# Performance work log

Measured on AMD Instinct MI355X. Metric: run time of the kernel, lower is better.

Reference implementation:

```python
import jax, jax.numpy as jnp
import numpy as np

B, HW, L, D = 4, 4096, 32, 128
H, DH = 2, 64            # heads, dim_head; inner_dim = H*DH = 128
SCALE = DH ** -0.5


def setup_inputs() -> dict:
    key = jax.random.key(0)
    ks = jax.random.split(key, 6)
    inner = H * DH
    return {
        "x": jax.random.normal(ks[0], (B, HW, 1, D), dtype=jnp.float32),
        "context": jax.random.normal(ks[1], (B, HW, L, D), dtype=jnp.float32),
        "Wq": jax.random.normal(ks[2], (D, inner), dtype=jnp.float32) * 0.02,
        "Wkv": jax.random.normal(ks[3], (D, 2 * inner), dtype=jnp.float32) * 0.02,
        "Wo": jax.random.normal(ks[4], (inner, D), dtype=jnp.float32) * 0.02,
        "bo": jnp.zeros((D,), dtype=jnp.float32),
    }


def reference(x, context, Wq, Wkv, Wo, bo):
    # q: [B, HW, 1, H*DH] -> [B, HW, H, DH] (single query per pixel)
    q = (x @ Wq).reshape(B, HW, H, DH)
    kv = context @ Wkv                       # [B, HW, L, 2*H*DH]
    k, v = jnp.split(kv, 2, axis=-1)
    k = k.reshape(B, HW, L, H, DH)
    v = v.reshape(B, HW, L, H, DH)
    # per-pixel 1xL attention, fused over (B, HW, H)
    sim = jnp.einsum('bphd,bplhd->bphl', q, k) * SCALE   # [B, HW, H, L]
    attn = jax.nn.softmax(sim, axis=-1)
    out = jnp.einsum('bphl,bplhd->bphd', attn, v)        # [B, HW, H, DH]
    out = out.reshape(B, HW, 1, H * DH)
    return out @ Wo + bo                                 # [B, HW, 1, D]
```

## Files before the change

kernel.cpp:

```cpp
#include <hip/hip_runtime.h>

#define NPIX 16384
#define LCTX 32
#define DIM  128
#define SCALE 0.125f

__global__ __launch_bounds__(256)
void fold_kernel(const float* __restrict__ Wq, const float* __restrict__ Wkv,
                 const float* __restrict__ Wo,
                 float* __restrict__ Ms, float* __restrict__ Nf)
{
    const int t = threadIdx.x;
    const int b = blockIdx.x;
    if (b < 128) {
        const int e = b, h = t >> 7, c = t & 127;
        const float4* q4p = reinterpret_cast<const float4*>(Wq + e * 128 + h * 64);
        const float4* k4p = reinterpret_cast<const float4*>(Wkv + c * 256 + h * 64);
        float acc = 0.f;
        #pragma unroll
        for (int d4 = 0; d4 < 16; ++d4) {
            const float4 a = q4p[d4], k = k4p[d4];
            acc += a.x * k.x + a.y * k.y + a.z * k.z + a.w * k.w;
        }
        Ms[e * 256 + t] = SCALE * acc;
    } else {
        const int b2 = b - 128;
        const int i = b2 * 2 + (t >> 7), j = t & 127;
        const int h = i >> 7, c = i & 127;
        const float4* v4p = reinterpret_cast<const float4*>(Wkv + c * 256 + 128 + h * 64);
        float acc = 0.f;
        #pragma unroll
        for (int d4 = 0; d4 < 16; ++d4) {
            const float4 v4 = v4p[d4];
            acc += v4.x * Wo[(h * 64 + d4 * 4 + 0) * 128 + j];
            acc += v4.y * Wo[(h * 64 + d4 * 4 + 1) * 128 + j];
            acc += v4.z * Wo[(h * 64 + d4 * 4 + 2) * 128 + j];
            acc += v4.w * Wo[(h * 64 + d4 * 4 + 3) * 128 + j];
        }
        Nf[i * 128 + j] = acc;
    }
}

__global__ __launch_bounds__(256, 4)
void fused_kernel(const float* __restrict__ x, const float* __restrict__ ctx,
                  const float* __restrict__ Ms, const float* __restrict__ Nf,
                  const float* __restrict__ bo, float* __restrict__ out)
{
    __shared__ float xs[16 * 128];
    __shared__ float cs[16 * 256];

    const int t = threadIdx.x;
    const int w = t >> 6, lane = t & 63;
    const int c0 = lane & 31;
    const int lh = lane >> 5;
    const int pxbase = blockIdx.x * 16;
    const int wpx = pxbase + w * 4;

    #pragma unroll
    for (int k = 0; k < 2; ++k)
        reinterpret_cast<float4*>(xs)[t + k * 256] =
            reinterpret_cast<const float4*>(x + (size_t)pxbase * DIM)[t + k * 256];
    __syncthreads();

    float4 qk4[4];
    #pragma unroll
    for (int p = 0; p < 4; ++p) qk4[p] = make_float4(0.f, 0.f, 0.f, 0.f);
    {
        const float4* ms4 = reinterpret_cast<const float4*>(Ms) + (lh * 32 + c0);
        const float4* xw  = reinterpret_cast<const float4*>(xs + (w * 4) * DIM);
        for (int e4 = 0; e4 < 32; ++e4) {
            float4 xv[4];
            #pragma unroll
            for (int p = 0; p < 4; ++p) xv[p] = xw[p * 32 + e4];
            #pragma unroll
            for (int d = 0; d < 4; ++d) {
                const float4 m4 = ms4[(e4 * 4 + d) * 64];
                #pragma unroll
                for (int p = 0; p < 4; ++p) {
                    const float xe = (d == 0) ? xv[p].x : (d == 1) ? xv[p].y
                                   : (d == 2) ? xv[p].z : xv[p].w;
                    qk4[p].x += xe * m4.x; qk4[p].y += xe * m4.y;
                    qk4[p].z += xe * m4.z; qk4[p].w += xe * m4.w;
                }
            }
        }
    }

    float m[4], dn[4];
    float4 acc[4];
    #pragma unroll
    for (int p = 0; p < 4; ++p) {
        m[p] = -3.0e38f; dn[p] = 0.f;
        acc[p] = make_float4(0.f, 0.f, 0.f, 0.f);
    }
    {
        const float4* cb0 = reinterpret_cast<const float4*>(ctx + (size_t)(wpx + 0) * LCTX * DIM) + c0;
        const float4* cb1 = reinterpret_cast<const float4*>(ctx + (size_t)(wpx + 1) * LCTX * DIM) + c0;
        const float4* cb2 = reinterpret_cast<const float4*>(ctx + (size_t)(wpx + 2) * LCTX * DIM) + c0;
        const float4* cb3 = reinterpret_cast<const float4*>(ctx + (size_t)(wpx + 3) * LCTX * DIM) + c0;
        #pragma unroll 4
        for (int r = 0; r < LCTX; ++r) {
            float4 cv[4];
            cv[0] = cb0[r * 32]; cv[1] = cb1[r * 32];
            cv[2] = cb2[r * 32]; cv[3] = cb3[r * 32];
            float part[4];
            #pragma unroll
            for (int p = 0; p < 4; ++p)
                part[p] = cv[p].x * qk4[p].x + cv[p].y * qk4[p].y
                        + cv[p].z * qk4[p].z + cv[p].w * qk4[p].w;
            #pragma unroll
            for (int off = 16; off >= 1; off >>= 1) {
                #pragma unroll
                for (int p = 0; p < 4; ++p) part[p] += __shfl_xor(part[p], off);
            }
            #pragma unroll
            for (int p = 0; p < 4; ++p) {
                const float mn = fmaxf(m[p], part[p]);
                const float sc = __expf(m[p] - mn);
                const float er = __expf(part[p] - mn);
                dn[p] = dn[p] * sc + er;
                acc[p].x = acc[p].x * sc + er * cv[p].x;
                acc[p].y = acc[p].y * sc + er * cv[p].y;
                acc[p].z = acc[p].z * sc + er * cv[p].z;
                acc[p].w = acc[p].w * sc + er * cv[p].w;
                m[p] = mn;
            }
        }
    }
    {
        float* csw = cs + (w * 4) * 256;
        #pragma unroll
        for (int p = 0; p < 4; ++p) {
            const float inv = 1.f / dn[p];
            float4 r = acc[p];
            r.x *= inv; r.y *= inv; r.z *= inv; r.w *= inv;
            reinterpret_cast<float4*>(csw + p * 256)[lh * 32 + c0] = r;
        }
    }

    {
        const int jq = lane & 31;
        const int ph = lane >> 5;
        const float4* csv0 = reinterpret_cast<const float4*>(cs + (w * 4 + ph * 2 + 0) * 256);
        const float4* csv1 = reinterpret_cast<const float4*>(cs + (w * 4 + ph * 2 + 1) * 256);
        const float4* nf4 = reinterpret_cast<const float4*>(Nf) + jq;
        float4 o0 = make_float4(0.f, 0.f, 0.f, 0.f);
        float4 o1 = make_float4(0.f, 0.f, 0.f, 0.f);
        #pragma unroll 4
        for (int i4 = 0; i4 < 64; ++i4) {
            const float4 a0 = csv0[i4];
            const float4 a1 = csv1[i4];
            #pragma unroll
            for (int d = 0; d < 4; ++d) {
                const float4 n4 = nf4[(i4 * 4 + d) * 32];
                const float a0e = (d == 0) ? a0.x : (d == 1) ? a0.y : (d == 2) ? a0.z : a0.w;
                const float a1e = (d == 0) ? a1.x : (d == 1) ? a1.y : (d == 2) ? a1.z : a1.w;
                o0.x += a0e * n4.x; o0.y += a0e * n4.y; o0.z += a0e * n4.z; o0.w += a0e * n4.w;
                o1.x += a1e * n4.x; o1.y += a1e * n4.y; o1.z += a1e * n4.z; o1.w += a1e * n4.w;
            }
        }
        const float4 b4 = reinterpret_cast<const float4*>(bo)[jq];
        o0.x += b4.x; o0.y += b4.y; o0.z += b4.z; o0.w += b4.w;
        o1.x += b4.x; o1.y += b4.y; o1.z += b4.z; o1.w += b4.w;
        reinterpret_cast<float4*>(out + (size_t)(wpx + ph * 2 + 0) * DIM)[jq] = o0;
        reinterpret_cast<float4*>(out + (size_t)(wpx + ph * 2 + 1) * DIM)[jq] = o1;
    }
}

#define PPB 8
__global__ __launch_bounds__(256, 4)
void ppca_kernel(const float* __restrict__ x, const float* __restrict__ ctx,
                 const float* __restrict__ Wq, const float* __restrict__ Wkv,
                 const float* __restrict__ Wo, const float* __restrict__ bo,
                 float* __restrict__ out)
{
    __shared__ float smem[4096];
    float* xs    = smem;
    float* qs    = smem + 1024;
    float* qks   = smem + 2048;
    float* attns = smem;
    float* ctxws = smem + 2048;
    float* outs  = smem + 1024;

    const int t = threadIdx.x;
    const int gbase = blockIdx.x * PPB;

    reinterpret_cast<float4*>(xs)[t] =
        reinterpret_cast<const float4*>(x + (size_t)gbase * DIM)[t];
    __syncthreads();

    {
        const int j = t & 127, pg = t >> 7;
        float acc[4] = {0.f, 0.f, 0.f, 0.f};
        for (int k = 0; k < 32; ++k) {
            const float w0 = Wq[(4*k + 0) * DIM + j];
            const float w1 = Wq[(4*k + 1) * DIM + j];
            const float w2 = Wq[(4*k + 2) * DIM + j];
            const float w3 = Wq[(4*k + 3) * DIM + j];
            #pragma unroll
            for (int pp = 0; pp < 4; ++pp) {
                const float4 xv = reinterpret_cast<const float4*>(xs + (pg*4 + pp) * DIM)[k];
                acc[pp] += xv.x*w0 + xv.y*w1 + xv.z*w2 + xv.w*w3;
            }
        }
        #pragma unroll
        for (int pp = 0; pp < 4; ++pp) qs[(pg*4 + pp) * DIM + j] = acc[pp];
    }
    __syncthreads();

    {
        const int c = t & 127, h = t >> 7;
        float acc[PPB] = {0.f,0.f,0.f,0.f,0.f,0.f,0.f,0.f};
        const float4* wrow = reinterpret_cast<const float4*>(Wkv + c * 256 + h * 64);
        for (int k = 0; k < 16; ++k) {
            const float4 w4 = wrow[k];
            #pragma unroll
            for (int p = 0; p < PPB; ++p) {
                const float4 q4 = reinterpret_cast<const float4*>(qs + p * DIM + h * 64)[k];
                acc[p] += q4.x*w4.x + q4.y*w4.y + q4.z*w4.z + q4.w*w4.w;
            }
        }
        #pragma unroll
        for (int p = 0; p < PPB; ++p) qks[(p*2 + h) * DIM + c] = acc[p];
    }
    __syncthreads();

    {
        const int l = t & 31, p = t >> 5;
        const float4* cr = reinterpret_cast<const float4*>(ctx + ((size_t)(gbase + p) * LCTX + l) * DIM);
        const float4* q0 = reinterpret_cast<const float4*>(qks + (p*2 + 0) * DIM);
        const float4* q1 = reinterpret_cast<const float4*>(qks + (p*2 + 1) * DIM);
        float s0 = 0.f, s1 = 0.f;
        #pragma unroll 8
        for (int k = 0; k < 32; ++k) {
            const float4 cv = cr[k], a = q0[k], b = q1[k];
            s0 += cv.x*a.x + cv.y*a.y + cv.z*a.z + cv.w*a.w;
            s1 += cv.x*b.x + cv.y*b.y + cv.z*b.z + cv.w*b.w;
        }
        s0 *= SCALE; s1 *= SCALE;
        float m0 = s0, m1 = s1;
        #pragma unroll
        for (int off = 16; off >= 1; off >>= 1) {
            m0 = fmaxf(m0, __shfl_xor(m0, off));
            m1 = fmaxf(m1, __shfl_xor(m1, off));
        }
        const float e0 = __expf(s0 - m0), e1 = __expf(s1 - m1);
        float d0 = e0, d1 = e1;
        #pragma unroll
        for (int off = 16; off >= 1; off >>= 1) {
            d0 += __shfl_xor(d0, off);
            d1 += __shfl_xor(d1, off);
        }
        attns[(p*2 + 0) * LCTX + l] = e0 / d0;
        attns[(p*2 + 1) * LCTX + l] = e1 / d1;
    }
    __syncthreads();

    {
        const int c = t & 127, pg = t >> 7;
        #pragma unroll
        for (int pp = 0; pp < 4; ++pp) {
            const int p = pg*4 + pp;
            const float* cb = ctx + (size_t)(gbase + p) * LCTX * DIM + c;
            const float4* a0p = reinterpret_cast<const float4*>(attns + (p*2 + 0) * LCTX);
            const float4* a1p = reinterpret_cast<const float4*>(attns + (p*2 + 1) * LCTX);
            float s0 = 0.f, s1 = 0.f;
            #pragma unroll
            for (int q = 0; q < 8; ++q) {
                const float4 a0 = a0p[q], a1 = a1p[q];
                const float c0 = cb[(size_t)(4*q + 0) * DIM];
                const float c1 = cb[(size_t)(4*q + 1) * DIM];
                const float c2 = cb[(size_t)(4*q + 2) * DIM];
                const float c3 = cb[(size_t)(4*q + 3) * DIM];
                s0 += a0.x*c0 + a0.y*c1 + a0.z*c2 + a0.w*c3;
                s1 += a1.x*c0 + a1.y*c1 + a1.z*c2 + a1.w*c3;
            }
            ctxws[(p*2 + 0) * DIM + c] = s0;
            ctxws[(p*2 + 1) * DIM + c] = s1;
        }
    }
    __syncthreads();

    {
        const int i = t & 127, pg = t >> 7, h = i >> 6;
        float acc[4] = {0.f, 0.f, 0.f, 0.f};
        for (int k = 0; k < 32; ++k) {
            const float w0 = Wkv[(4*k + 0) * 256 + 128 + i];
            const float w1 = Wkv[(4*k + 1) * 256 + 128 + i];
            const float w2 = Wkv[(4*k + 2) * 256 + 128 + i];
            const float w3 = Wkv[(4*k + 3) * 256 + 128 + i];
            #pragma unroll
            for (int pp = 0; pp < 4; ++pp) {
                const float4 cw = reinterpret_cast<const float4*>(ctxws + ((pg*4 + pp)*2 + h) * DIM)[k];
                acc[pp] += cw.x*w0 + cw.y*w1 + cw.z*w2 + cw.w*w3;
            }
        }
        #pragma unroll
        for (int pp = 0; pp < 4; ++pp) outs[(pg*4 + pp) * DIM + i] = acc[pp];
    }
    __syncthreads();

    {
        const int j = t & 127, pg = t >> 7;
        float acc[4] = {0.f, 0.f, 0.f, 0.f};
        for (int k = 0; k < 32; ++k) {
            const float w0 = Wo[(4*k + 0) * DIM + j];
            const float w1 = Wo[(4*k + 1) * DIM + j];
            const float w2 = Wo[(4*k + 2) * DIM + j];
            const float w3 = Wo[(4*k + 3) * DIM + j];
            #pragma unroll
            for (int pp = 0; pp < 4; ++pp) {
                const float4 ov = reinterpret_cast<const float4*>(outs + (pg*4 + pp) * DIM)[k];
                acc[pp] += ov.x*w0 + ov.y*w1 + ov.z*w2 + ov.w*w3;
            }
        }
        const float bj = bo[j];
        #pragma unroll
        for (int pp = 0; pp < 4; ++pp)
            out[(size_t)(gbase + pg*4 + pp) * DIM + j] = acc[pp] + bj;
    }
}

extern "C" void kernel_launch(void* const* d_in, const int* in_sizes, int n_in,
                              void* d_out, int out_size, void* d_ws, size_t ws_size,
                              hipStream_t stream) {
    const float* x   = (const float*)d_in[0];
    const float* ctx = (const float*)d_in[1];
    const float* Wq  = (const float*)d_in[2];
    const float* Wkv = (const float*)d_in[3];
    const float* Wo  = (const float*)d_in[4];
    const float* bo  = (const float*)d_in[5];
    float* out = (float*)d_out;

    const size_t needed = (size_t)(32768 + 32768) * sizeof(float);
    if (ws_size < needed) {
        dim3 grid(NPIX / PPB), block(256);
        hipLaunchKernelGGL(ppca_kernel, grid, block, 0, stream,
                           x, ctx, Wq, Wkv, Wo, bo, out);
        return;
    }

    float* Ms = (float*)d_ws;
    float* Nf = Ms + 32768;

    hipLaunchKernelGGL(fold_kernel,  dim3(256),  dim3(256), 0, stream, Wq, Wkv, Wo, Ms, Nf);
    hipLaunchKernelGGL(fused_kernel, dim3(NPIX / 16), dim3(256), 0, stream,
                       x, ctx, Ms, Nf, bo, out);
}
```

Baseline: 117.5 us.

## Restructure fused attention kernel to process one pixel at a time per wave

```diff
diff --git a/kernel.cpp b/kernel.cpp
--- a/kernel.cpp
+++ b/kernel.cpp
@@ -4,6 +4,7 @@
 #define LCTX 32
 #define DIM  128
 #define SCALE 0.125f
+#define PXW  4
 
 __global__ __launch_bounds__(256)
 void fold_kernel(const float* __restrict__ Wq, const float* __restrict__ Wkv,
@@ -42,41 +43,33 @@
 }
 
 __global__ __launch_bounds__(256, 4)
-void fused_kernel(const float* __restrict__ x, const float* __restrict__ ctx,
-                  const float* __restrict__ Ms, const float* __restrict__ Nf,
-                  const float* __restrict__ bo, float* __restrict__ out)
+void fused2_kernel(const float* __restrict__ x, const float* __restrict__ ctx,
+                   const float* __restrict__ Ms, const float* __restrict__ Nf,
+                   const float* __restrict__ bo, float* __restrict__ out)
 {
-    __shared__ float xs[16 * 128];
-    __shared__ float cs[16 * 256];
+    __shared__ float cw[4][PXW * 256];
 
     const int t = threadIdx.x;
     const int w = t >> 6, lane = t & 63;
     const int c0 = lane & 31;
-    const int lh = lane >> 5;
-    const int pxbase = blockIdx.x * 16;
-    const int wpx = pxbase + w * 4;
-
+    const int wpx = (blockIdx.x * 4 + w) * PXW;
+
+    float4 qk4[PXW];
     #pragma unroll
-    for (int k = 0; k < 2; ++k)
-        reinterpret_cast<float4*>(xs)[t + k * 256] =
-            reinterpret_cast<const float4*>(x + (size_t)pxbase * DIM)[t + k * 256];
-    __syncthreads();
-
-    float4 qk4[4];
-    #pragma unroll
-    for (int p = 0; p < 4; ++p) qk4[p] = make_float4(0.f, 0.f, 0.f, 0.f);
-    {
-        const float4* ms4 = reinterpret_cast<const float4*>(Ms) + (lh * 32 + c0);
-        const float4* xw  = reinterpret_cast<const float4*>(xs + (w * 4) * DIM);
+    for (int p = 0; p < PXW; ++p) qk4[p] = make_float4(0.f, 0.f, 0.f, 0.f);
+    {
+        const float4* ms4 = reinterpret_cast<const float4*>(Ms) + lane;
+        #pragma unroll 4
         for (int e4 = 0; e4 < 32; ++e4) {
-            float4 xv[4];
-            #pragma unroll
-            for (int p = 0; p < 4; ++p) xv[p] = xw[p * 32 + e4];
+            float4 xv[PXW];
+            #pragma unroll
+            for (int p = 0; p < PXW; ++p)
+                xv[p] = reinterpret_cast<const float4*>(x + (size_t)(wpx + p) * DIM)[e4];
             #pragma unroll
             for (int d = 0; d < 4; ++d) {
                 const float4 m4 = ms4[(e4 * 4 + d) * 64];
                 #pragma unroll
-                for (int p = 0; p < 4; ++p) {
+                for (int p = 0; p < PXW; ++p) {
                     const float xe = (d == 0) ? xv[p].x : (d == 1) ? xv[p].y
                                    : (d == 2) ? xv[p].z : xv[p].w;
                     qk4[p].x += xe * m4.x; qk4[p].y += xe * m4.y;
@@ -86,84 +79,75 @@
         }
     }
 
-    float m[4], dn[4];
-    float4 acc[4];
     #pragma unroll
-    for (int p = 0; p < 4; ++p) {
-        m[p] = -3.0e38f; dn[p] = 0.f;
-        acc[p] = make_float4(0.f, 0.f, 0.f, 0.f);
-    }
-    {
-        const float4* cb0 = reinterpret_cast<const float4*>(ctx + (size_t)(wpx + 0) * LCTX * DIM) + c0;
-        const float4* cb1 = reinterpret_cast<const float4*>(ctx + (size_t)(wpx + 1) * LCTX * DIM) + c0;
-        const float4* cb2 = reinterpret_cast<const float4*>(ctx + (size_t)(wpx + 2) * LCTX * DIM) + c0;
-        const float4* cb3 = reinterpret_cast<const float4*>(ctx + (size_t)(wpx + 3) * LCTX * DIM) + c0;
-        #pragma unroll 4
+    for (int p = 0; p < PXW; ++p) {
+        const float4* cb =
+            reinterpret_cast<const float4*>(ctx + (size_t)(wpx + p) * LCTX * DIM) + c0;
+
+        float sim[LCTX];
+        #pragma unroll
         for (int r = 0; r < LCTX; ++r) {
-            float4 cv[4];
-            cv[0] = cb0[r * 32]; cv[1] = cb1[r * 32];
-            cv[2] = cb2[r * 32]; cv[3] = cb3[r * 32];
-            float part[4];
-            #pragma unroll
-            for (int p = 0; p < 4; ++p)
-                part[p] = cv[p].x * qk4[p].x + cv[p].y * qk4[p].y
-                        + cv[p].z * qk4[p].z + cv[p].w * qk4[p].w;
-            #pragma unroll
-            for (int off = 16; off >= 1; off >>= 1) {
+            const float4 cv = cb[r * 32];
+            float part = cv.x * qk4[p].x + cv.y * qk4[p].y
+                       + cv.z * qk4[p].z + cv.w * qk4[p].w;
+            #pragma unroll
+            for (int off = 16; off >= 1; off >>= 1) part += __shfl_xor(part, off);
+            sim[r] = part;
+        }
+
+        float mx = sim[0];
+        #pragma unroll
+        for (int r = 1; r < LCTX; ++r) mx = fmaxf(mx, sim[r]);
+        float dn = 0.f;
+        #pragma unroll
+        for (int r = 0; r < LCTX; ++r) { sim[r] = __expf(sim[r] - mx); dn += sim[r]; }
+        const float inv = 1.f / dn;
+
+        uintptr_t ub = (uintptr_t)cb;
+        asm volatile("" : "+v"(ub));
+        const float4* cbB = (const float4*)ub;
+
+        float4 acc = make_float4(0.f, 0.f, 0.f, 0.f);
+        #pragma unroll
+        for (int r = 0; r < LCTX; ++r) {
+            const float4 cv = cbB[r * 32];
+            const float a = sim[r] * inv;
+            acc.x += a * cv.x; acc.y += a * cv.y;
+            acc.z += a * cv.z; acc.w += a * cv.w;
+        }
+        reinterpret_cast<float4*>(&cw[w][p * 256])[lane] = acc;
+    }
+
+    {
+        const float2* nf2 = reinterpret_cast<const float2*>(Nf) + lane;
+        const float2  b2  = reinterpret_cast<const float2*>(bo)[lane];
+        float2 o[PXW];
+        #pragma unroll
+        for (int p = 0; p < PXW; ++p) o[p] = make_float2(0.f, 0.f);
+
+        #pragma unroll 2
+        for (int i4 = 0; i4 < 64; ++i4) {
+            float4 a4[PXW];
+            #pragma unroll
+            for (int p = 0; p < PXW; ++p)
+                a4[p] = reinterpret_cast<const float4*>(&cw[w][p * 256])[i4];
+            #pragma unroll
+            for (int d = 0; d < 4; ++d) {
+                const float2 n2 = nf2[(i4 * 4 + d) * 64];
                 #pragma unroll
-                for (int p = 0; p < 4; ++p) part[p] += __shfl_xor(part[p], off);
-            }
-            #pragma unroll
-            for (int p = 0; p < 4; ++p) {
-                const float mn = fmaxf(m[p], part[p]);
-                const float sc = __expf(m[p] - mn);
-                const float er = __expf(part[p] - mn);
-                dn[p] = dn[p] * sc + er;
-                acc[p].x = acc[p].x * sc + er * cv[p].x;
-                acc[p].y = acc[p].y * sc + er * cv[p].y;
-                acc[p].z = acc[p].z * sc + er * cv[p].z;
-                acc[p].w = acc[p].w * sc + er * cv[p].w;
-                m[p] = mn;
-            }
-        }
-    }
-    {
-        float* csw = cs + (w * 4) * 256;
-        #pragma unroll
-        for (int p = 0; p < 4; ++p) {
-            const float inv = 1.f / dn[p];
-            float4 r = acc[p];
-            r.x *= inv; r.y *= inv; r.z *= inv; r.w *= inv;
-            reinterpret_cast<float4*>(csw + p * 256)[lh * 32 + c0] = r;
-        }
-    }
-
-    {
-        const int jq = lane & 31;
-        const int ph = lane >> 5;
-        const float4* csv0 = reinterpret_cast<const float4*>(cs + (w * 4 + ph * 2 + 0) * 256);
-        const float4* csv1 = reinterpret_cast<const float4*>(cs + (w * 4 + ph * 2 + 1) * 256);
-        const float4* nf4 = reinterpret_cast<const float4*>(Nf) + jq;
-        float4 o0 = make_float4(0.f, 0.f, 0.f, 0.f);
-        float4 o1 = make_float4(0.f, 0.f, 0.f, 0.f);
-        #pragma unroll 4
-        for (int i4 = 0; i4 < 64; ++i4) {
-            const float4 a0 = csv0[i4];
-            const float4 a1 = csv1[i4];
-            #pragma unroll
-            for (int d = 0; d < 4; ++d) {
-                const float4 n4 = nf4[(i4 * 4 + d) * 32];
-                const float a0e = (d == 0) ? a0.x : (d == 1) ? a0.y : (d == 2) ? a0.z : a0.w;
-                const float a1e = (d == 0) ? a1.x : (d == 1) ? a1.y : (d == 2) ? a1.z : a1.w;
-                o0.x += a0e * n4.x; o0.y += a0e * n4.y; o0.z += a0e * n4.z; o0.w += a0e * n4.w;
-                o1.x += a1e * n4.x; o1.y += a1e * n4.y; o1.z += a1e * n4.z; o1.w += a1e * n4.w;
-            }
-        }
-        const float4 b4 = reinterpret_cast<const float4*>(bo)[jq];
-        o0.x += b4.x; o0.y += b4.y; o0.z += b4.z; o0.w += b4.w;
-        o1.x += b4.x; o1.y += b4.y; o1.z += b4.z; o1.w += b4.w;
-        reinterpret_cast<float4*>(out + (size_t)(wpx + ph * 2 + 0) * DIM)[jq] = o0;
-        reinterpret_cast<float4*>(out + (size_t)(wpx + ph * 2 + 1) * DIM)[jq] = o1;
+                for (int p = 0; p < PXW; ++p) {
+                    const float ae = (d == 0) ? a4[p].x : (d == 1) ? a4[p].y
+                                   : (d == 2) ? a4[p].z : a4[p].w;
+                    o[p].x += ae * n2.x; o[p].y += ae * n2.y;
+                }
+            }
+        }
+        #pragma unroll
+        for (int p = 0; p < PXW; ++p) {
+            float2 r = o[p];
+            r.x += b2.x; r.y += b2.y;
+            reinterpret_cast<float2*>(out + (size_t)(wpx + p) * DIM)[lane] = r;
+        }
     }
 }
 
@@ -291,8 +275,8 @@
             const float w3 = Wkv[(4*k + 3) * 256 + 128 + i];
             #pragma unroll
             for (int pp = 0; pp < 4; ++pp) {
-                const float4 cw = reinterpret_cast<const float4*>(ctxws + ((pg*4 + pp)*2 + h) * DIM)[k];
-                acc[pp] += cw.x*w0 + cw.y*w1 + cw.z*w2 + cw.w*w3;
+                const float4 cw4 = reinterpret_cast<const float4*>(ctxws + ((pg*4 + pp)*2 + h) * DIM)[k];
+                acc[pp] += cw4.x*w0 + cw4.y*w1 + cw4.z*w2 + cw4.w*w3;
             }
         }
         #pragma unroll
@@ -343,7 +327,7 @@
     float* Ms = (float*)d_ws;
     float* Nf = Ms + 32768;
 
-    hipLaunchKernelGGL(fold_kernel,  dim3(256),  dim3(256), 0, stream, Wq, Wkv, Wo, Ms, Nf);
-    hipLaunchKernelGGL(fused_kernel, dim3(NPIX / 16), dim3(256), 0, stream,
+    hipLaunchKernelGGL(fold_kernel,  dim3(256), dim3(256), 0, stream, Wq, Wkv, Wo, Ms, Nf);
+    hipLaunchKernelGGL(fused2_kernel, dim3(NPIX / (4 * PXW)), dim3(256), 0, stream,
                        x, ctx, Ms, Nf, bo, out);
 }
```

Result: slower. 124.2 us (+5.7%).
